# Kernel tuning notes

Hardware: AMD Instinct MI355X
Metric: run time of the kernel (lower is better)

The kernel has to match this reference:

```python
import jax, jax.numpy as jnp
import numpy as np

B, U, V, C = 2, 8, 512, 256
H, DK = 8, 64            # num_heads, key_query_features (per head)
R = 256                  # result_features; per-head value dim R//H = 32
CODE = 192
EPS = 1e-6               # affinity renorm epsilon
LN_EPS = 1e-5            # torch LayerNorm default
GAIN = 2.5               # post_attention_gain / post_mlp_gain buffers


def _ln(x, g, b):
    m = x.mean(-1, keepdims=True)
    v = ((x - m) ** 2).mean(-1, keepdims=True)
    return (x - m) / jnp.sqrt(v + LN_EPS) * g + b


def _modlin(x, c, W, Wc, b=None):
    # ModFC / ModLin: y = W(x * (1 + Wc c)) (+ b)
    y = (x * (1.0 + c @ Wc)) @ W
    return y if b is None else y + b


def setup_inputs() -> dict:
    key = jax.random.key(0)
    ks = jax.random.split(key, 16)
    s = 0.02
    return {
        'variables': jax.random.normal(ks[0], (B, U, V, C), jnp.float32),
        'codes': jax.random.normal(ks[1], (U, CODE), jnp.float32),
        'affinities': jax.random.uniform(ks[2], (B, U, V), jnp.float32),
        'ln1_g': jnp.ones((C,), jnp.float32),
        'ln1_b': jnp.zeros((C,), jnp.float32),
        'Wq': jax.random.normal(ks[3], (C, H * DK), jnp.float32) * s,
        'Wcq': jax.random.normal(ks[4], (CODE, C), jnp.float32) * s,
        'Wk': jax.random.normal(ks[5], (C, H * DK), jnp.float32) * s,
        'Wck': jax.random.normal(ks[6], (CODE, C), jnp.float32) * s,
        'Wv': jax.random.normal(ks[7], (C, R), jnp.float32) * s,
        'Wcv': jax.random.normal(ks[8], (CODE, C), jnp.float32) * s,
        'bv': jnp.zeros((R,), jnp.float32),
        'ln2_g': jnp.ones((R,), jnp.float32),
        'ln2_b': jnp.zeros((R,), jnp.float32),
        'W1': jax.random.normal(ks[9], (R, R), jnp.float32) * s,
        'Wc1': jax.random.normal(ks[10], (CODE, R), jnp.float32) * s,
        'b1m': jnp.zeros((R,), jnp.float32),
        'W2': jax.random.normal(ks[11], (R, R), jnp.float32) * s,
        'Wc2': jax.random.normal(ks[12], (CODE, R), jnp.float32) * s,
        'b2m': jnp.zeros((R,), jnp.float32),
    }


def reference(variables, codes, affinities, ln1_g, ln1_b, Wq, Wcq, Wk, Wck,
              Wv, Wcv, bv, ln2_g, ln2_b, W1, Wc1, b1m, W2, Wc2, b2m):
    # codes: [U, code] -> broadcast to [B, U, V, code]
    c4 = jnp.broadcast_to(codes[None, :, None, :], (B, U, V, CODE))
    xn = _ln(variables, ln1_g, ln1_b)                      # b u v c
    q = _modlin(xn, c4, Wq, Wcq).reshape(B, U, V, H, DK)   # b u v h d
    k = _modlin(xn, c4, Wk, Wck).reshape(B, U, V, H, DK)
    v = _modlin(xn, c4, Wv, Wcv, bv).reshape(B, U, V, H, R // H)
    # scores: b u r s h (attention over s); scale_attention_weights=False -> scale 1
    scores = jnp.einsum('burhd,bushd->bursh', q, k)
    dot = jax.nn.softmax(scores, axis=3)                   # softmax over s (dim=-2)
    # affinity modulation: aff_r * aff_s * weights, renormalized over s
    kmw = affinities[:, :, :, None, None] * affinities[:, :, None, :, None] * dot
    kmw = kmw / (kmw.sum(axis=3, keepdims=True) + EPS)
    att = jnp.einsum('bursh,bushc->burhc', kmw, v).reshape(B, U, V, R)
    g = affinities[..., None]
    # residual_mode='gating', variable_features==result_features
    attn_out = (1.0 - g) * variables + g * GAIN * att
    yn = _ln(attn_out, ln2_g, ln2_b)
    h1 = jax.nn.gelu(_modlin(yn, c4, W1, Wc1, b1m), approximate=False)
    h2 = jax.nn.gelu(_modlin(h1, c4, W2, Wc2, b2m), approximate=False)
    mlp_out = h2 * g
    results = (1.0 - g) * attn_out + g * GAIN * mlp_out
    return results
```

## Files before the change

### kernel.cpp

```cpp
#include <hip/hip_runtime.h>
#include <math.h>

#define B_ 2
#define U_ 8
#define V_ 512
#define C_ 256
#define H_ 8
#define R_ 256
#define EPS_ 1e-6f
#define LN_EPS_ 1e-5f
#define GAIN_ 2.5f

typedef __attribute__((ext_vector_type(8))) short bf16x8;
typedef __attribute__((ext_vector_type(4))) float f32x4;
typedef unsigned short ushort_t;

__device__ __forceinline__ ushort_t f2bf(float x) {
    union { float f; unsigned u; } v; v.f = x;
    unsigned r = v.u + 0x7fffu + ((v.u >> 16) & 1u);
    return (ushort_t)(r >> 16);
}

__device__ __forceinline__ float waveReduceSum(float v) {
    #pragma unroll
    for (int m = 1; m < 64; m <<= 1) v += __shfl_xor(v, m);
    return v;
}

__device__ __forceinline__ float gelu_exact(float x) {
    return 0.5f * x * (1.f + erff(x * 0.70710678118654752f));
}

__global__ void k_mods(const float* __restrict__ codes,
                       const float* __restrict__ Wcq, const float* __restrict__ Wck,
                       const float* __restrict__ Wcv, const float* __restrict__ Wc1,
                       const float* __restrict__ Wc2, const float* __restrict__ bv,
                       float* __restrict__ mods, float* __restrict__ biasQ) {
    int id = blockIdx.x;
    int kind = id >> 3, u = id & 7;
    const float* Wc = (kind == 0) ? Wcq : (kind == 1) ? Wck :
                      (kind == 2) ? Wcv : (kind == 3) ? Wc1 : Wc2;
    int c = threadIdx.x;
    const float* cd = codes + u * 192;
    float a = 0.f;
    for (int j = 0; j < 192; ++j) a = fmaf(cd[j], Wc[j * 256 + c], a);
    mods[id * 256 + c] = 1.f + a;
    if (id == 0) {
        biasQ[c] = 0.f; biasQ[256 + c] = 0.f; biasQ[512 + c] = 0.f;
        biasQ[768 + c] = 0.f; biasQ[1024 + c] = bv[c];
    }
}

__global__ __launch_bounds__(256) void k_fold(
    const float* __restrict__ Wq, const float* __restrict__ Wk,
    const float* __restrict__ Wv, const float* __restrict__ W1,
    const float* __restrict__ W2, const float* __restrict__ mods,
    ushort_t* __restrict__ wqkvT, ushort_t* __restrict__ w1T,
    ushort_t* __restrict__ w2T) {
    __shared__ ushort_t T[64][65];
    int id = blockIdx.x;
    const float* W; int ldw, modIdx, colAdd, tilesPerU, base;
    ushort_t* dst; int dstCols;
    if (id < 256)      { base = 0;   W = Wq; ldw = 512; modIdx = 0; colAdd = 0;    dst = wqkvT; dstCols = 1280; tilesPerU = 32; }
    else if (id < 512) { base = 256; W = Wk; ldw = 512; modIdx = 1; colAdd = 512;  dst = wqkvT; dstCols = 1280; tilesPerU = 32; }
    else if (id < 640) { base = 512; W = Wv; ldw = 256; modIdx = 2; colAdd = 1024; dst = wqkvT; dstCols = 1280; tilesPerU = 16; }
    else if (id < 768) { base = 640; W = W1; ldw = 256; modIdx = 3; colAdd = 0;    dst = w1T;  dstCols = 256;  tilesPerU = 16; }
    else               { base = 768; W = W2; ldw = 256; modIdx = 4; colAdd = 0;    dst = w2T;  dstCols = 256;  tilesPerU = 16; }
    int local = id - base;
    int u = local / tilesPerU;
    int t = local % tilesPerU;
    int nColTiles = ldw / 64;
    int c0 = (t / nColTiles) * 64;
    int col0 = (t % nColTiles) * 64;
    const float* modRow = mods + (modIdx * U_ + u) * C_;
    int tid = threadIdx.x;
    int cl = tid >> 4;
    int cg = (tid & 15) * 4;
    #pragma unroll
    for (int it = 0; it < 4; ++it) {
        int c = cl + it * 16;
        float m = modRow[c0 + c];
        float4 wv = *(const float4*)&W[(size_t)(c0 + c) * ldw + col0 + cg];
        T[c][cg + 0] = f2bf(wv.x * m);
        T[c][cg + 1] = f2bf(wv.y * m);
        T[c][cg + 2] = f2bf(wv.z * m);
        T[c][cg + 3] = f2bf(wv.w * m);
    }
    __syncthreads();
    int j = tid >> 2;
    int ch = (tid & 3) * 16;
    ushort_t tmp[16];
    #pragma unroll
    for (int i = 0; i < 16; ++i) tmp[i] = T[ch + i][j];
    ushort_t* o = dst + ((size_t)u * dstCols + colAdd + col0 + j) * 256 + c0 + ch;
    *(bf16x8*)&o[0] = *(const bf16x8*)&tmp[0];
    *(bf16x8*)&o[8] = *(const bf16x8*)&tmp[8];
}

__global__ void k_ln1(const float* __restrict__ x, const float* __restrict__ g,
                      const float* __restrict__ b, ushort_t* __restrict__ xnb) {
    int row = blockIdx.x * 4 + (threadIdx.x >> 6);
    int lane = threadIdx.x & 63;
    const float* xr = x + (size_t)row * C_;
    float4 v = *(const float4*)&xr[lane * 4];
    float s = v.x + v.y + v.z + v.w;
    float ss = v.x * v.x + v.y * v.y + v.z * v.z + v.w * v.w;
    s = waveReduceSum(s); ss = waveReduceSum(ss);
    float mean = s * (1.f / 256.f);
    float var = ss * (1.f / 256.f) - mean * mean;
    float rstd = rsqrtf(var + LN_EPS_);
    float4 gg = *(const float4*)&g[lane * 4];
    float4 bb = *(const float4*)&b[lane * 4];
    unsigned lo = (unsigned)f2bf((v.x - mean) * rstd * gg.x + bb.x)
                | ((unsigned)f2bf((v.y - mean) * rstd * gg.y + bb.y) << 16);
    unsigned hi = (unsigned)f2bf((v.z - mean) * rstd * gg.z + bb.z)
                | ((unsigned)f2bf((v.w - mean) * rstd * gg.w + bb.w) << 16);
    uint2 pk; pk.x = lo; pk.y = hi;
    *(uint2*)&xnb[(size_t)row * C_ + lane * 4] = pk;
}

__global__ __launch_bounds__(256) void k_qkv(
    const ushort_t* __restrict__ X, const ushort_t* __restrict__ WT,
    const float* __restrict__ biasQ, ushort_t* __restrict__ out,
    ushort_t* __restrict__ vT) {
    __shared__ __align__(16) ushort_t xs[128][72];
    __shared__ __align__(16) ushort_t wt[128][72];
    int col0 = blockIdx.x * 128;
    int row0 = blockIdx.y * 128;
    int u = (row0 >> 9) & 7;
    const ushort_t* Wu = WT + (size_t)(u * 1280 + col0) * 256;
    int tid = threadIdx.x;
    int w = tid >> 6, l = tid & 63;
    int lr = l & 15, lg = l >> 4;
    int wm = w >> 1, wn = w & 1;
    f32x4 acc[4][4] = {};
    int sr = tid >> 3, sko = (tid & 7) * 8;
    for (int k0 = 0; k0 < 256; k0 += 64) {
        #pragma unroll
        for (int it = 0; it < 4; ++it) {
            int r = sr + it * 32;
            *(bf16x8*)&xs[r][sko] = *(const bf16x8*)&X[(size_t)(row0 + r) * 256 + k0 + sko];
            *(bf16x8*)&wt[r][sko] = *(const bf16x8*)&Wu[(size_t)r * 256 + k0 + sko];
        }
        __syncthreads();
        #pragma unroll
        for (int m = 0; m < 4; ++m) {
            #pragma unroll
            for (int kk = 0; kk < 2; ++kk) {
                bf16x8 a = *(const bf16x8*)&xs[wm * 64 + m * 16 + lr][kk * 32 + lg * 8];
                #pragma unroll
                for (int n = 0; n < 4; ++n) {
                    bf16x8 bb = *(const bf16x8*)&wt[wn * 64 + n * 16 + lr][kk * 32 + lg * 8];
                    acc[m][n] = __builtin_amdgcn_mfma_f32_16x16x32_bf16(a, bb, acc[m][n], 0, 0, 0);
                }
            }
        }
        __syncthreads();
    }
    #pragma unroll
    for (int m = 0; m < 4; ++m) {
        int rowb = row0 + wm * 64 + m * 16 + lg * 4;
        #pragma unroll
        for (int n = 0; n < 4; ++n) {
            int col = col0 + wn * 64 + n * 16 + lr;
            float bval = biasQ[col];
            ushort_t pk4[4];
            #pragma unroll
            for (int i = 0; i < 4; ++i) {
                float v = acc[m][n][i] + bval;
                pk4[i] = f2bf(v);
                out[(size_t)(rowb + i) * 1280 + col] = pk4[i];
            }
            if (col >= 1024) {
                int hh = (col - 1024) >> 5, cc = (col - 1024) & 31;
                int bu = rowb >> 9;
                uint2 pw;
                pw.x = (unsigned)pk4[0] | ((unsigned)pk4[1] << 16);
                pw.y = (unsigned)pk4[2] | ((unsigned)pk4[3] << 16);
                *(uint2*)&vT[(size_t)((bu * 8 + hh) * 32 + cc) * 512 + (rowb & 511)] = pw;
            }
        }
    }
}

__global__ __launch_bounds__(256) void k_attn(
    const ushort_t* __restrict__ qkv, const ushort_t* __restrict__ vT,
    const float* __restrict__ aff, float* __restrict__ att) {
    __shared__ __align__(16) ushort_t Qs[64][72];
    __shared__ __align__(16) ushort_t Ks[64][72];
    __shared__ __align__(16) ushort_t Pt[64][72];
    __shared__ __align__(16) ushort_t Vt[32][72];
    __shared__ float As[64];
    int id = blockIdx.x;
    int xcd = id & 7, sl = id >> 3;
    int bu = xcd + 8 * (sl >> 6);
    int inr = sl & 63;
    int h = inr & 7;
    int r0 = (inr >> 3) * 64;
    const ushort_t* base = qkv + (size_t)bu * 512 * 1280;
    const ushort_t* vbase = vT + (size_t)((bu * 8 + h) * 32) * 512;
    int tid = threadIdx.x;
    int w = tid >> 6, l = tid & 63;
    int lr = l & 15, lg = l >> 4;
    int sr = tid >> 3, sko = (tid & 7) * 8;
    *(bf16x8*)&Qs[sr][sko]      = *(const bf16x8*)&base[(size_t)(r0 + sr) * 1280 + h * 64 + sko];
    *(bf16x8*)&Qs[sr + 32][sko] = *(const bf16x8*)&base[(size_t)(r0 + sr + 32) * 1280 + h * 64 + sko];
    bf16x8 kr0 = *(const bf16x8*)&base[(size_t)sr * 1280 + 512 + h * 64 + sko];
    bf16x8 kr1 = *(const bf16x8*)&base[(size_t)(sr + 32) * 1280 + 512 + h * 64 + sko];
    bf16x8 vr  = *(const bf16x8*)&vbase[(size_t)sr * 512 + sko];
    float afv = (tid < 64) ? aff[bu * 512 + tid] : 0.f;
    *(bf16x8*)&Ks[sr][sko] = kr0;
    *(bf16x8*)&Ks[sr + 32][sko] = kr1;
    if (sr < 32) *(bf16x8*)&Vt[sr][sko] = vr;
    if (tid < 64) As[tid] = afv;
    __syncthreads();
    float wsum = 0.f, asum = 0.f;
    f32x4 pacc[2] = {};
    for (int t = 0; t < 8; ++t) {
        int s0n = (t + 1) * 64;
        if (t < 7) {
            kr0 = *(const bf16x8*)&base[(size_t)(s0n + sr) * 1280 + 512 + h * 64 + sko];
            kr1 = *(const bf16x8*)&base[(size_t)(s0n + sr + 32) * 1280 + 512 + h * 64 + sko];
            if (sr < 32) vr = *(const bf16x8*)&vbase[(size_t)sr * 512 + s0n + sko];
            if (tid < 64) afv = aff[bu * 512 + s0n + tid];
        }
        #pragma unroll
        for (int n = 0; n < 4; ++n) {
            f32x4 sc = {};
            #pragma unroll
            for (int kk = 0; kk < 2; ++kk) {
                bf16x8 ka = *(const bf16x8*)&Ks[n * 16 + lr][kk * 32 + lg * 8];
                bf16x8 qb = *(const bf16x8*)&Qs[w * 16 + lr][kk * 32 + lg * 8];
                sc = __builtin_amdgcn_mfma_f32_16x16x32_bf16(ka, qb, sc, 0, 0, 0);
            }
            float4 a4 = *(const float4*)&As[n * 16 + lg * 4];
            float e0 = __expf(sc[0]), e1 = __expf(sc[1]);
            float e2 = __expf(sc[2]), e3 = __expf(sc[3]);
            wsum += (e0 + e1) + (e2 + e3);
            float ae0 = e0 * a4.x, ae1 = e1 * a4.y, ae2 = e2 * a4.z, ae3 = e3 * a4.w;
            asum += (ae0 + ae1) + (ae2 + ae3);
            uint2 pw;
            pw.x = (unsigned)f2bf(ae0) | ((unsigned)f2bf(ae1) << 16);
            pw.y = (unsigned)f2bf(ae2) | ((unsigned)f2bf(ae3) << 16);
            *(uint2*)&Pt[w * 16 + lr][n * 16 + lg * 4] = pw;
        }
        #pragma unroll
        for (int n = 0; n < 2; ++n) {
            #pragma unroll
            for (int kk = 0; kk < 2; ++kk) {
                bf16x8 pa = *(const bf16x8*)&Pt[w * 16 + lr][kk * 32 + lg * 8];
                bf16x8 vb = *(const bf16x8*)&Vt[n * 16 + lr][kk * 32 + lg * 8];
                pacc[n] = __builtin_amdgcn_mfma_f32_16x16x32_bf16(pa, vb, pacc[n], 0, 0, 0);
            }
        }
        __syncthreads();
        if (t < 7) {
            *(bf16x8*)&Ks[sr][sko] = kr0;
            *(bf16x8*)&Ks[sr + 32][sko] = kr1;
            if (sr < 32) *(bf16x8*)&Vt[sr][sko] = vr;
            if (tid < 64) As[tid] = afv;
            __syncthreads();
        }
    }
    asum += __shfl_xor(asum, 16); asum += __shfl_xor(asum, 32);
    wsum += __shfl_xor(wsum, 16); wsum += __shfl_xor(wsum, 32);
    float ar = aff[bu * 512 + r0 + w * 16 + lr];
    float scale = ar / (ar * asum + EPS_ * wsum);
    #pragma unroll
    for (int i = 0; i < 4; ++i) {
        float sc_i = __shfl(scale, lg * 4 + i);
        int q = r0 + w * 16 + lg * 4 + i;
        float* ob = att + ((size_t)bu * 512 + q) * 256 + h * 32;
        ob[lr]      = pacc[0][i] * sc_i;
        ob[16 + lr] = pacc[1][i] * sc_i;
    }
}

__global__ void k_gate_ln2(const float* __restrict__ x, const float* __restrict__ att,
                           const float* __restrict__ aff, const float* __restrict__ g2,
                           const float* __restrict__ b2, float* __restrict__ ao,
                           ushort_t* __restrict__ ynb) {
    int row = blockIdx.x * 4 + (threadIdx.x >> 6);
    int lane = threadIdx.x & 63;
    float a = aff[row];
    const float* xr = x + (size_t)row * C_;
    const float* atr = att + (size_t)row * C_;
    float4 xv = *(const float4*)&xr[lane * 4];
    float4 av = *(const float4*)&atr[lane * 4];
    float4 o;
    o.x = (1.f - a) * xv.x + a * GAIN_ * av.x;
    o.y = (1.f - a) * xv.y + a * GAIN_ * av.y;
    o.z = (1.f - a) * xv.z + a * GAIN_ * av.z;
    o.w = (1.f - a) * xv.w + a * GAIN_ * av.w;
    float s = o.x + o.y + o.z + o.w;
    float ss = o.x * o.x + o.y * o.y + o.z * o.z + o.w * o.w;
    s = waveReduceSum(s); ss = waveReduceSum(ss);
    float mean = s * (1.f / 256.f);
    float var = ss * (1.f / 256.f) - mean * mean;
    float rstd = rsqrtf(var + LN_EPS_);
    *(float4*)&ao[(size_t)row * C_ + lane * 4] = o;
    float4 gg = *(const float4*)&g2[lane * 4];
    float4 bb = *(const float4*)&b2[lane * 4];
    unsigned lo = (unsigned)f2bf((o.x - mean) * rstd * gg.x + bb.x)
                | ((unsigned)f2bf((o.y - mean) * rstd * gg.y + bb.y) << 16);
    unsigned hi = (unsigned)f2bf((o.z - mean) * rstd * gg.z + bb.z)
                | ((unsigned)f2bf((o.w - mean) * rstd * gg.w + bb.w) << 16);
    uint2 pk; pk.x = lo; pk.y = hi;
    *(uint2*)&ynb[(size_t)row * C_ + lane * 4] = pk;
}

template<int MODE>
__global__ __launch_bounds__(256) void k_gemm(
    const ushort_t* __restrict__ X, const ushort_t* __restrict__ WT, int wPerU,
    const float* __restrict__ bias, ushort_t* __restrict__ outB, int ldo,
    float* __restrict__ outF, const float* __restrict__ ao,
    const float* __restrict__ aff) {
    __shared__ __align__(16) ushort_t xs[64][72];
    __shared__ __align__(16) ushort_t wt[64][72];
    int col0 = blockIdx.x * 64;
    int row0 = blockIdx.y * 64;
    int u = (row0 >> 9) & 7;
    const ushort_t* Wu = WT + ((size_t)u * wPerU + col0) * 256;
    int tid = threadIdx.x;
    int w = tid >> 6, l = tid & 63;
    int lr = l & 15, lg = l >> 4;
    f32x4 acc[4] = {};
    for (int k0 = 0; k0 < 256; k0 += 64) {
        int r1 = tid >> 3, ko1 = (tid & 7) * 8;
        int r2 = (tid + 256) >> 3, ko2 = ((tid + 256) & 7) * 8;
        *(bf16x8*)&xs[r1][ko1] = *(const bf16x8*)&X[(size_t)(row0 + r1) * 256 + k0 + ko1];
        *(bf16x8*)&xs[r2][ko2] = *(const bf16x8*)&X[(size_t)(row0 + r2) * 256 + k0 + ko2];
        *(bf16x8*)&wt[r1][ko1] = *(const bf16x8*)&Wu[(size_t)r1 * 256 + k0 + ko1];
        *(bf16x8*)&wt[r2][ko2] = *(const bf16x8*)&Wu[(size_t)r2 * 256 + k0 + ko2];
        __syncthreads();
        #pragma unroll
        for (int n = 0; n < 4; ++n) {
            #pragma unroll
            for (int kk = 0; kk < 2; ++kk) {
                bf16x8 a = *(const bf16x8*)&xs[w * 16 + lr][kk * 32 + lg * 8];
                bf16x8 bb = *(const bf16x8*)&wt[n * 16 + lr][kk * 32 + lg * 8];
                acc[n] = __builtin_amdgcn_mfma_f32_16x16x32_bf16(a, bb, acc[n], 0, 0, 0);
            }
        }
        __syncthreads();
    }
    #pragma unroll
    for (int n = 0; n < 4; ++n) {
        int col = col0 + n * 16 + lr;
        float bval = bias[col];
        #pragma unroll
        for (int i = 0; i < 4; ++i) {
            int row = row0 + w * 16 + lg * 4 + i;
            float v = gelu_exact(acc[n][i] + bval);
            if (MODE == 2) {
                float a = aff[row];
                float aov = ao[(size_t)row * 256 + col];
                outF[(size_t)row * 256 + col] = (1.f - a) * aov + GAIN_ * a * a * v;
            } else {
                outB[(size_t)row * ldo + col] = f2bf(v);
            }
        }
    }
}

extern "C" void kernel_launch(void* const* d_in, const int* in_sizes, int n_in,
                              void* d_out, int out_size, void* d_ws, size_t ws_size,
                              hipStream_t stream) {
    const float* variables  = (const float*)d_in[0];
    const float* codes      = (const float*)d_in[1];
    const float* affinities = (const float*)d_in[2];
    const float* ln1_g = (const float*)d_in[3];
    const float* ln1_b = (const float*)d_in[4];
    const float* Wq  = (const float*)d_in[5];
    const float* Wcq = (const float*)d_in[6];
    const float* Wk  = (const float*)d_in[7];
    const float* Wck = (const float*)d_in[8];
    const float* Wv  = (const float*)d_in[9];
    const float* Wcv = (const float*)d_in[10];
    const float* bv  = (const float*)d_in[11];
    const float* ln2_g = (const float*)d_in[12];
    const float* ln2_b = (const float*)d_in[13];
    const float* W1  = (const float*)d_in[14];
    const float* Wc1 = (const float*)d_in[15];
    const float* b1m = (const float*)d_in[16];
    const float* W2  = (const float*)d_in[17];
    const float* Wc2 = (const float*)d_in[18];
    const float* b2m = (const float*)d_in[19];

    char* p = (char*)d_ws;
    float* modsF = (float*)p;   p += 40960;
    float* biasQ = (float*)p;   p += 5120;
    float* attF  = (float*)p;   p += 8388608;
    float* aoF   = (float*)p;   p += 8388608;
    ushort_t* xnb   = (ushort_t*)p; p += 4194304;
    ushort_t* wqkvT = (ushort_t*)p; p += 5242880;
    ushort_t* w1T   = (ushort_t*)p; p += 1048576;
    ushort_t* w2T   = (ushort_t*)p; p += 1048576;
    ushort_t* qkvb  = (ushort_t*)p; p += 20971520;
    ushort_t* ynb   = (ushort_t*)p; p += 4194304;
    ushort_t* h1b   = (ushort_t*)p; p += 4194304;
    ushort_t* vTb   = (ushort_t*)p; p += 4194304;
    float* outp = (float*)d_out;

    k_mods<<<40, 256, 0, stream>>>(codes, Wcq, Wck, Wcv, Wc1, Wc2, bv, modsF, biasQ);
    k_fold<<<896, 256, 0, stream>>>(Wq, Wk, Wv, W1, W2, modsF, wqkvT, w1T, w2T);
    k_ln1<<<2048, 256, 0, stream>>>(variables, ln1_g, ln1_b, xnb);
    k_qkv<<<dim3(10, 64), 256, 0, stream>>>(xnb, wqkvT, biasQ, qkvb, vTb);
    k_attn<<<1024, 256, 0, stream>>>(qkvb, vTb, affinities, attF);
    k_gate_ln2<<<2048, 256, 0, stream>>>(variables, attF, affinities, ln2_g, ln2_b, aoF, ynb);
    k_gemm<1><<<dim3(4, 128), 256, 0, stream>>>(ynb, w1T, 256, b1m, h1b, 256,
                                                nullptr, nullptr, nullptr);
    k_gemm<2><<<dim3(4, 128), 256, 0, stream>>>(h1b, w2T, 256, b2m, nullptr, 256,
                                                outp, aoF, affinities);
}
```

Baseline: 175.6 us.

## Fuse prep kernels and the gate/LN2/MLP tail into single kernels

```diff
diff --git a/kernel.cpp b/kernel.cpp
--- a/kernel.cpp
+++ b/kernel.cpp
@@ -31,34 +31,45 @@
     return 0.5f * x * (1.f + erff(x * 0.70710678118654752f));
 }
 
-__global__ void k_mods(const float* __restrict__ codes,
-                       const float* __restrict__ Wcq, const float* __restrict__ Wck,
-                       const float* __restrict__ Wcv, const float* __restrict__ Wc1,
-                       const float* __restrict__ Wc2, const float* __restrict__ bv,
-                       float* __restrict__ mods, float* __restrict__ biasQ) {
-    int id = blockIdx.x;
-    int kind = id >> 3, u = id & 7;
-    const float* Wc = (kind == 0) ? Wcq : (kind == 1) ? Wck :
-                      (kind == 2) ? Wcv : (kind == 3) ? Wc1 : Wc2;
-    int c = threadIdx.x;
-    const float* cd = codes + u * 192;
-    float a = 0.f;
-    for (int j = 0; j < 192; ++j) a = fmaf(cd[j], Wc[j * 256 + c], a);
-    mods[id * 256 + c] = 1.f + a;
-    if (id == 0) {
-        biasQ[c] = 0.f; biasQ[256 + c] = 0.f; biasQ[512 + c] = 0.f;
-        biasQ[768 + c] = 0.f; biasQ[1024 + c] = bv[c];
-    }
-}
-
-__global__ __launch_bounds__(256) void k_fold(
+__global__ __launch_bounds__(256) void k_prep(
+    const float* __restrict__ codes,
+    const float* __restrict__ Wcq, const float* __restrict__ Wck,
+    const float* __restrict__ Wcv, const float* __restrict__ Wc1,
+    const float* __restrict__ Wc2,
     const float* __restrict__ Wq, const float* __restrict__ Wk,
     const float* __restrict__ Wv, const float* __restrict__ W1,
-    const float* __restrict__ W2, const float* __restrict__ mods,
+    const float* __restrict__ W2,
+    const float* __restrict__ x, const float* __restrict__ ln1g,
+    const float* __restrict__ ln1b,
     ushort_t* __restrict__ wqkvT, ushort_t* __restrict__ w1T,
-    ushort_t* __restrict__ w2T) {
+    ushort_t* __restrict__ w2T, ushort_t* __restrict__ xnb) {
+    int bid = blockIdx.x;
+    int tid = threadIdx.x;
+    if (bid >= 896) {
+        int row = (bid - 896) * 4 + (tid >> 6);
+        int lane = tid & 63;
+        const float* xr = x + (size_t)row * C_;
+        float4 v = *(const float4*)&xr[lane * 4];
+        float s = v.x + v.y + v.z + v.w;
+        float ss = v.x * v.x + v.y * v.y + v.z * v.z + v.w * v.w;
+        s = waveReduceSum(s); ss = waveReduceSum(ss);
+        float mean = s * (1.f / 256.f);
+        float var = ss * (1.f / 256.f) - mean * mean;
+        float rstd = rsqrtf(var + LN_EPS_);
+        float4 gg = *(const float4*)&ln1g[lane * 4];
+        float4 bb = *(const float4*)&ln1b[lane * 4];
+        unsigned lo = (unsigned)f2bf((v.x - mean) * rstd * gg.x + bb.x)
+                    | ((unsigned)f2bf((v.y - mean) * rstd * gg.y + bb.y) << 16);
+        unsigned hi = (unsigned)f2bf((v.z - mean) * rstd * gg.z + bb.z)
+                    | ((unsigned)f2bf((v.w - mean) * rstd * gg.w + bb.w) << 16);
+        uint2 pk; pk.x = lo; pk.y = hi;
+        *(uint2*)&xnb[(size_t)row * C_ + lane * 4] = pk;
+        return;
+    }
+    __shared__ float mpart[4][64];
+    __shared__ float mrow[64];
     __shared__ ushort_t T[64][65];
-    int id = blockIdx.x;
+    int id = bid;
     const float* W; int ldw, modIdx, colAdd, tilesPerU, base;
     ushort_t* dst; int dstCols;
     if (id < 256)      { base = 0;   W = Wq; ldw = 512; modIdx = 0; colAdd = 0;    dst = wqkvT; dstCols = 1280; tilesPerU = 32; }
@@ -66,20 +77,35 @@
     else if (id < 640) { base = 512; W = Wv; ldw = 256; modIdx = 2; colAdd = 1024; dst = wqkvT; dstCols = 1280; tilesPerU = 16; }
     else if (id < 768) { base = 640; W = W1; ldw = 256; modIdx = 3; colAdd = 0;    dst = w1T;  dstCols = 256;  tilesPerU = 16; }
     else               { base = 768; W = W2; ldw = 256; modIdx = 4; colAdd = 0;    dst = w2T;  dstCols = 256;  tilesPerU = 16; }
+    const float* Wc = (modIdx == 0) ? Wcq : (modIdx == 1) ? Wck :
+                      (modIdx == 2) ? Wcv : (modIdx == 3) ? Wc1 : Wc2;
     int local = id - base;
     int u = local / tilesPerU;
     int t = local % tilesPerU;
     int nColTiles = ldw / 64;
     int c0 = (t / nColTiles) * 64;
     int col0 = (t % nColTiles) * 64;
-    const float* modRow = mods + (modIdx * U_ + u) * C_;
-    int tid = threadIdx.x;
+    {
+        const float* cd = codes + u * 192;
+        int cc = tid & 63, g = tid >> 6;
+        float accm = 0.f;
+        #pragma unroll 4
+        for (int jj = 0; jj < 48; ++jj) {
+            int j = g * 48 + jj;
+            accm = fmaf(cd[j], Wc[j * 256 + c0 + cc], accm);
+        }
+        mpart[g][cc] = accm;
+        __syncthreads();
+        if (tid < 64)
+            mrow[tid] = 1.f + mpart[0][tid] + mpart[1][tid] + mpart[2][tid] + mpart[3][tid];
+        __syncthreads();
+    }
     int cl = tid >> 4;
     int cg = (tid & 15) * 4;
     #pragma unroll
     for (int it = 0; it < 4; ++it) {
         int c = cl + it * 16;
-        float m = modRow[c0 + c];
+        float m = mrow[c];
         float4 wv = *(const float4*)&W[(size_t)(c0 + c) * ldw + col0 + cg];
         T[c][cg + 0] = f2bf(wv.x * m);
         T[c][cg + 1] = f2bf(wv.y * m);
@@ -97,31 +123,9 @@
     *(bf16x8*)&o[8] = *(const bf16x8*)&tmp[8];
 }
 
-__global__ void k_ln1(const float* __restrict__ x, const float* __restrict__ g,
-                      const float* __restrict__ b, ushort_t* __restrict__ xnb) {
-    int row = blockIdx.x * 4 + (threadIdx.x >> 6);
-    int lane = threadIdx.x & 63;
-    const float* xr = x + (size_t)row * C_;
-    float4 v = *(const float4*)&xr[lane * 4];
-    float s = v.x + v.y + v.z + v.w;
-    float ss = v.x * v.x + v.y * v.y + v.z * v.z + v.w * v.w;
-    s = waveReduceSum(s); ss = waveReduceSum(ss);
-    float mean = s * (1.f / 256.f);
-    float var = ss * (1.f / 256.f) - mean * mean;
-    float rstd = rsqrtf(var + LN_EPS_);
-    float4 gg = *(const float4*)&g[lane * 4];
-    float4 bb = *(const float4*)&b[lane * 4];
-    unsigned lo = (unsigned)f2bf((v.x - mean) * rstd * gg.x + bb.x)
-                | ((unsigned)f2bf((v.y - mean) * rstd * gg.y + bb.y) << 16);
-    unsigned hi = (unsigned)f2bf((v.z - mean) * rstd * gg.z + bb.z)
-                | ((unsigned)f2bf((v.w - mean) * rstd * gg.w + bb.w) << 16);
-    uint2 pk; pk.x = lo; pk.y = hi;
-    *(uint2*)&xnb[(size_t)row * C_ + lane * 4] = pk;
-}
-
 __global__ __launch_bounds__(256) void k_qkv(
     const ushort_t* __restrict__ X, const ushort_t* __restrict__ WT,
-    const float* __restrict__ biasQ, ushort_t* __restrict__ out,
+    const float* __restrict__ bv, ushort_t* __restrict__ out,
     ushort_t* __restrict__ vT) {
     __shared__ __align__(16) ushort_t xs[128][72];
     __shared__ __align__(16) ushort_t wt[128][72];
@@ -163,7 +167,7 @@
         #pragma unroll
         for (int n = 0; n < 4; ++n) {
             int col = col0 + wn * 64 + n * 16 + lr;
-            float bval = biasQ[col];
+            float bval = (col >= 1024) ? bv[col - 1024] : 0.f;
             ushort_t pk4[4];
             #pragma unroll
             for (int i = 0; i < 4; ++i) {
@@ -276,90 +280,139 @@
     }
 }
 
-__global__ void k_gate_ln2(const float* __restrict__ x, const float* __restrict__ att,
-                           const float* __restrict__ aff, const float* __restrict__ g2,
-                           const float* __restrict__ b2, float* __restrict__ ao,
-                           ushort_t* __restrict__ ynb) {
-    int row = blockIdx.x * 4 + (threadIdx.x >> 6);
-    int lane = threadIdx.x & 63;
-    float a = aff[row];
-    const float* xr = x + (size_t)row * C_;
-    const float* atr = att + (size_t)row * C_;
-    float4 xv = *(const float4*)&xr[lane * 4];
-    float4 av = *(const float4*)&atr[lane * 4];
-    float4 o;
-    o.x = (1.f - a) * xv.x + a * GAIN_ * av.x;
-    o.y = (1.f - a) * xv.y + a * GAIN_ * av.y;
-    o.z = (1.f - a) * xv.z + a * GAIN_ * av.z;
-    o.w = (1.f - a) * xv.w + a * GAIN_ * av.w;
-    float s = o.x + o.y + o.z + o.w;
-    float ss = o.x * o.x + o.y * o.y + o.z * o.z + o.w * o.w;
-    s = waveReduceSum(s); ss = waveReduceSum(ss);
-    float mean = s * (1.f / 256.f);
-    float var = ss * (1.f / 256.f) - mean * mean;
-    float rstd = rsqrtf(var + LN_EPS_);
-    *(float4*)&ao[(size_t)row * C_ + lane * 4] = o;
-    float4 gg = *(const float4*)&g2[lane * 4];
-    float4 bb = *(const float4*)&b2[lane * 4];
-    unsigned lo = (unsigned)f2bf((o.x - mean) * rstd * gg.x + bb.x)
-                | ((unsigned)f2bf((o.y - mean) * rstd * gg.y + bb.y) << 16);
-    unsigned hi = (unsigned)f2bf((o.z - mean) * rstd * gg.z + bb.z)
-                | ((unsigned)f2bf((o.w - mean) * rstd * gg.w + bb.w) << 16);
-    uint2 pk; pk.x = lo; pk.y = hi;
-    *(uint2*)&ynb[(size_t)row * C_ + lane * 4] = pk;
-}
-
-template<int MODE>
-__global__ __launch_bounds__(256) void k_gemm(
-    const ushort_t* __restrict__ X, const ushort_t* __restrict__ WT, int wPerU,
-    const float* __restrict__ bias, ushort_t* __restrict__ outB, int ldo,
-    float* __restrict__ outF, const float* __restrict__ ao,
-    const float* __restrict__ aff) {
-    __shared__ __align__(16) ushort_t xs[64][72];
-    __shared__ __align__(16) ushort_t wt[64][72];
-    int col0 = blockIdx.x * 64;
-    int row0 = blockIdx.y * 64;
-    int u = (row0 >> 9) & 7;
-    const ushort_t* Wu = WT + ((size_t)u * wPerU + col0) * 256;
+__global__ __launch_bounds__(256) void k_tail(
+    const float* __restrict__ x, const float* __restrict__ att,
+    const float* __restrict__ aff, const float* __restrict__ g2,
+    const float* __restrict__ b2, const ushort_t* __restrict__ w1T,
+    const ushort_t* __restrict__ w2T, const float* __restrict__ b1m,
+    const float* __restrict__ b2m, float* __restrict__ outp) {
+    __shared__ __align__(16) ushort_t yn[32][264];
+    __shared__ __align__(16) ushort_t wt[256][72];
+    int r0 = blockIdx.x * 32;
+    int u = (r0 >> 9) & 7;
     int tid = threadIdx.x;
-    int w = tid >> 6, l = tid & 63;
-    int lr = l & 15, lg = l >> 4;
-    f32x4 acc[4] = {};
+    {
+        int row = tid >> 3, cb = (tid & 7) * 32;
+        float a = aff[r0 + row];
+        const float* xr = x + (size_t)(r0 + row) * 256 + cb;
+        const float* ar = att + (size_t)(r0 + row) * 256 + cb;
+        float4 o[8];
+        float s = 0.f, ss = 0.f;
+        #pragma unroll
+        for (int j = 0; j < 8; ++j) {
+            float4 xv = *(const float4*)&xr[j * 4];
+            float4 av = *(const float4*)&ar[j * 4];
+            float4 t;
+            t.x = (1.f - a) * xv.x + a * GAIN_ * av.x;
+            t.y = (1.f - a) * xv.y + a * GAIN_ * av.y;
+            t.z = (1.f - a) * xv.z + a * GAIN_ * av.z;
+            t.w = (1.f - a) * xv.w + a * GAIN_ * av.w;
+            o[j] = t;
+            s += (t.x + t.y) + (t.z + t.w);
+            ss += (t.x * t.x + t.y * t.y) + (t.z * t.z + t.w * t.w);
+        }
+        s += __shfl_xor(s, 1); s += __shfl_xor(s, 2); s += __shfl_xor(s, 4);
+        ss += __shfl_xor(ss, 1); ss += __shfl_xor(ss, 2); ss += __shfl_xor(ss, 4);
+        float mean = s * (1.f / 256.f);
+        float var = ss * (1.f / 256.f) - mean * mean;
+        float rstd = rsqrtf(var + LN_EPS_);
+        #pragma unroll
+        for (int j = 0; j < 8; ++j) {
+            float4 gg = *(const float4*)&g2[cb + j * 4];
+            float4 bb = *(const float4*)&b2[cb + j * 4];
+            uint2 pk;
+            pk.x = (unsigned)f2bf((o[j].x - mean) * rstd * gg.x + bb.x)
+                 | ((unsigned)f2bf((o[j].y - mean) * rstd * gg.y + bb.y) << 16);
+            pk.y = (unsigned)f2bf((o[j].z - mean) * rstd * gg.z + bb.z)
+                 | ((unsigned)f2bf((o[j].w - mean) * rstd * gg.w + bb.w) << 16);
+            *(uint2*)&yn[row][cb + j * 4] = pk;
+        }
+    }
+    __syncthreads();
+    int w = tid >> 6, l = tid & 63, lr = l & 15, lg = l >> 4;
+    int tokT = w & 1, nh = w >> 1;
+    int scol = tid >> 3, sko = (tid & 7) * 8;
+    const ushort_t* W1u = w1T + (size_t)u * 256 * 256;
+    const ushort_t* W2u = w2T + (size_t)u * 256 * 256;
+    f32x4 acc[8] = {};
     for (int k0 = 0; k0 < 256; k0 += 64) {
-        int r1 = tid >> 3, ko1 = (tid & 7) * 8;
-        int r2 = (tid + 256) >> 3, ko2 = ((tid + 256) & 7) * 8;
-        *(bf16x8*)&xs[r1][ko1] = *(const bf16x8*)&X[(size_t)(row0 + r1) * 256 + k0 + ko1];
-        *(bf16x8*)&xs[r2][ko2] = *(const bf16x8*)&X[(size_t)(row0 + r2) * 256 + k0 + ko2];
-        *(bf16x8*)&wt[r1][ko1] = *(const bf16x8*)&Wu[(size_t)r1 * 256 + k0 + ko1];
-        *(bf16x8*)&wt[r2][ko2] = *(const bf16x8*)&Wu[(size_t)r2 * 256 + k0 + ko2];
-        __syncthreads();
-        #pragma unroll
-        for (int n = 0; n < 4; ++n) {
+        #pragma unroll
+        for (int it = 0; it < 8; ++it)
+            *(bf16x8*)&wt[scol + it * 32][sko] =
+                *(const bf16x8*)&W1u[(size_t)(scol + it * 32) * 256 + k0 + sko];
+        __syncthreads();
+        #pragma unroll
+        for (int n = 0; n < 8; ++n) {
             #pragma unroll
             for (int kk = 0; kk < 2; ++kk) {
-                bf16x8 a = *(const bf16x8*)&xs[w * 16 + lr][kk * 32 + lg * 8];
-                bf16x8 bb = *(const bf16x8*)&wt[n * 16 + lr][kk * 32 + lg * 8];
-                acc[n] = __builtin_amdgcn_mfma_f32_16x16x32_bf16(a, bb, acc[n], 0, 0, 0);
-            }
-        }
-        __syncthreads();
-    }
-    #pragma unroll
-    for (int n = 0; n < 4; ++n) {
-        int col = col0 + n * 16 + lr;
-        float bval = bias[col];
-        #pragma unroll
-        for (int i = 0; i < 4; ++i) {
-            int row = row0 + w * 16 + lg * 4 + i;
-            float v = gelu_exact(acc[n][i] + bval);
-            if (MODE == 2) {
-                float a = aff[row];
-                float aov = ao[(size_t)row * 256 + col];
-                outF[(size_t)row * 256 + col] = (1.f - a) * aov + GAIN_ * a * a * v;
-            } else {
-                outB[(size_t)row * ldo + col] = f2bf(v);
-            }
-        }
+                bf16x8 a = *(const bf16x8*)&wt[(nh * 8 + n) * 16 + lr][kk * 32 + lg * 8];
+                bf16x8 b = *(const bf16x8*)&yn[tokT * 16 + lr][k0 + kk * 32 + lg * 8];
+                acc[n] = __builtin_amdgcn_mfma_f32_16x16x32_bf16(a, b, acc[n], 0, 0, 0);
+            }
+        }
+        __syncthreads();
+    }
+    #pragma unroll
+    for (int n = 0; n < 8; ++n) {
+        int nc = (nh * 8 + n) * 16 + lg * 4;
+        float4 bv1 = *(const float4*)&b1m[nc];
+        ushort_t p0 = f2bf(gelu_exact(acc[n][0] + bv1.x));
+        ushort_t p1 = f2bf(gelu_exact(acc[n][1] + bv1.y));
+        ushort_t p2 = f2bf(gelu_exact(acc[n][2] + bv1.z));
+        ushort_t p3 = f2bf(gelu_exact(acc[n][3] + bv1.w));
+        uint2 pw;
+        pw.x = (unsigned)p0 | ((unsigned)p1 << 16);
+        pw.y = (unsigned)p2 | ((unsigned)p3 << 16);
+        *(uint2*)&yn[tokT * 16 + lr][nc] = pw;
+    }
+    f32x4 acc2[8] = {};
+    for (int k0 = 0; k0 < 256; k0 += 64) {
+        #pragma unroll
+        for (int it = 0; it < 8; ++it)
+            *(bf16x8*)&wt[scol + it * 32][sko] =
+                *(const bf16x8*)&W2u[(size_t)(scol + it * 32) * 256 + k0 + sko];
+        __syncthreads();
+        #pragma unroll
+        for (int n = 0; n < 8; ++n) {
+            #pragma unroll
+            for (int kk = 0; kk < 2; ++kk) {
+                bf16x8 a = *(const bf16x8*)&wt[(nh * 8 + n) * 16 + lr][kk * 32 + lg * 8];
+                bf16x8 b = *(const bf16x8*)&yn[tokT * 16 + lr][k0 + kk * 32 + lg * 8];
+                acc2[n] = __builtin_amdgcn_mfma_f32_16x16x32_bf16(a, b, acc2[n], 0, 0, 0);
+            }
+        }
+        __syncthreads();
+    }
+    int orow = r0 + tokT * 16 + lr;
+    float a = aff[orow];
+    #pragma unroll
+    for (int n = 0; n < 8; ++n) {
+        int nc = (nh * 8 + n) * 16 + lg * 4;
+        float4 bv2 = *(const float4*)&b2m[nc];
+        float4 xv = *(const float4*)&x[(size_t)orow * 256 + nc];
+        float4 av = *(const float4*)&att[(size_t)orow * 256 + nc];
+        float4 r;
+        {
+            float h2 = gelu_exact(acc2[n][0] + bv2.x);
+            float ao = (1.f - a) * xv.x + a * GAIN_ * av.x;
+            r.x = (1.f - a) * ao + GAIN_ * a * a * h2;
+        }
+        {
+            float h2 = gelu_exact(acc2[n][1] + bv2.y);
+            float ao = (1.f - a) * xv.y + a * GAIN_ * av.y;
+            r.y = (1.f - a) * ao + GAIN_ * a * a * h2;
+        }
+        {
+            float h2 = gelu_exact(acc2[n][2] + bv2.z);
+            float ao = (1.f - a) * xv.z + a * GAIN_ * av.z;
+            r.z = (1.f - a) * ao + GAIN_ * a * a * h2;
+        }
+        {
+            float h2 = gelu_exact(acc2[n][3] + bv2.w);
+            float ao = (1.f - a) * xv.w + a * GAIN_ * av.w;
+            r.w = (1.f - a) * ao + GAIN_ * a * a * h2;
+        }
+        *(float4*)&outp[(size_t)orow * 256 + nc] = r;
     }
 }
 
@@ -388,28 +441,21 @@
     const float* b2m = (const float*)d_in[19];
 
     char* p = (char*)d_ws;
-    float* modsF = (float*)p;   p += 40960;
-    float* biasQ = (float*)p;   p += 5120;
-    float* attF  = (float*)p;   p += 8388608;
-    float* aoF   = (float*)p;   p += 8388608;
+    float* attF     = (float*)p;    p += 8388608;
     ushort_t* xnb   = (ushort_t*)p; p += 4194304;
     ushort_t* wqkvT = (ushort_t*)p; p += 5242880;
     ushort_t* w1T   = (ushort_t*)p; p += 1048576;
     ushort_t* w2T   = (ushort_t*)p; p += 1048576;
     ushort_t* qkvb  = (ushort_t*)p; p += 20971520;
-    ushort_t* ynb   = (ushort_t*)p; p += 4194304;
-    ushort_t* h1b   = (ushort_t*)p; p += 4194304;
     ushort_t* vTb   = (ushort_t*)p; p += 4194304;
     float* outp = (float*)d_out;
 
-    k_mods<<<40, 256, 0, stream>>>(codes, Wcq, Wck, Wcv, Wc1, Wc2, bv, modsF, biasQ);
-    k_fold<<<896, 256, 0, stream>>>(Wq, Wk, Wv, W1, W2, modsF, wqkvT, w1T, w2T);
-    k_ln1<<<2048, 256, 0, stream>>>(variables, ln1_g, ln1_b, xnb);
-    k_qkv<<<dim3(10, 64), 256, 0, stream>>>(xnb, wqkvT, biasQ, qkvb, vTb);
+    k_prep<<<2944, 256, 0, stream>>>(codes, Wcq, Wck, Wcv, Wc1, Wc2,
+                                     Wq, Wk, Wv, W1, W2,
+                                     variables, ln1_g, ln1_b,
+                                     wqkvT, w1T, w2T, xnb);
+    k_qkv<<<dim3(10, 64), 256, 0, stream>>>(xnb, wqkvT, bv, qkvb, vTb);
     k_attn<<<1024, 256, 0, stream>>>(qkvb, vTb, affinities, attF);
-    k_gate_ln2<<<2048, 256, 0, stream>>>(variables, attF, affinities, ln2_g, ln2_b, aoF, ynb);
-    k_gemm<1><<<dim3(4, 128), 256, 0, stream>>>(ynb, w1T, 256, b1m, h1b, 256,
-                                                nullptr, nullptr, nullptr);
-    k_gemm<2><<<dim3(4, 128), 256, 0, stream>>>(h1b, w2T, 256, b2m, nullptr, 256,
-                                                outp, aoF, affinities);
-}
+    k_tail<<<256, 256, 0, stream>>>(variables, attF, affinities, ln2_g, ln2_b,
+                                    w1T, w2T, b1m, b2m, outp);
+}
```

Measured after the change: 166.8 us. 1.05x faster.
